# Performance work log

Hardware: AMD Instinct MI355X
Metric: run time of the kernel (lower is better)

The kernel has to match this reference:

```python
import jax, jax.numpy as jnp
import numpy as np


def setup_inputs() -> dict:
    key = jax.random.key(0)
    k1, k2, k3 = jax.random.split(key, 3)
    B, C, H, W = 8, 512, 32, 32
    x = jax.random.normal(k1, (B, C, H, W), dtype=jnp.float32)
    # Conv2d(ch, ch, 3, 1, 1) weights, PyTorch OIHW layout
    fan_in = C * 3 * 3
    weight = jax.random.normal(k2, (C, C, 3, 3), dtype=jnp.float32) / np.sqrt(fan_in)
    bias = jax.random.normal(k3, (C,), dtype=jnp.float32) * 0.01
    return {"x": x, "weight": weight, "bias": bias}


def reference(x, weight, bias):
    up = jnp.repeat(jnp.repeat(x, 2, axis=2), 2, axis=3)
    # Conv3x3, stride 1, padding 1 (same spatial size)
    out = jax.lax.conv_general_dilated(
        up, weight,
        window_strides=(1, 1),
        padding=((1, 1), (1, 1)),
        dimension_numbers=("NCHW", "OIHW", "NCHW"),
    )
    return out + bias[None, :, None, None]
```

## Files before the change

kernel.cpp:

```cpp
#include <hip/hip_runtime.h>
#include <hip/hip_bf16.h>
#include <stdint.h>


typedef __attribute__((ext_vector_type(8)))  __bf16 bf16x8;
typedef __attribute__((ext_vector_type(4)))  float  f32x4;
typedef __attribute__((ext_vector_type(4)))  int    int4v;

__device__ __forceinline__ void async16(const void* g, void* l) {
  __builtin_amdgcn_global_load_lds(
      (const __attribute__((address_space(1))) void*)g,
      (__attribute__((address_space(3))) void*)l,
      16, 0, 0);
}

__global__ void fused_prep(const float* __restrict__ x,
                           const float* __restrict__ w,
                           __hip_bfloat16* __restrict__ xpad,
                           __hip_bfloat16* __restrict__ weff) {
  const int bid = blockIdx.x;
  const int tid = threadIdx.x;
  __shared__ __align__(16) __hip_bfloat16 ldsT[32][80];

  if (bid < 2048) {
    const int blk = bid;
    const int cib = blk & 7;
    const int r   = (blk >> 3) & 31;
    const int b   = blk >> 8;
    const int ci_l = tid >> 2;
    const int wq   = tid & 3;
    const float* xp = x + (((size_t)(b * 512 + cib * 64 + ci_l) * 32 + r) * 32) + wq * 8;
    float4 v0 = *(const float4*)(xp);
    float4 v1 = *(const float4*)(xp + 4);
    const int wb = wq * 8;
    ldsT[wb + 0][ci_l] = __float2bfloat16(v0.x);
    ldsT[wb + 1][ci_l] = __float2bfloat16(v0.y);
    ldsT[wb + 2][ci_l] = __float2bfloat16(v0.z);
    ldsT[wb + 3][ci_l] = __float2bfloat16(v0.w);
    ldsT[wb + 4][ci_l] = __float2bfloat16(v1.x);
    ldsT[wb + 5][ci_l] = __float2bfloat16(v1.y);
    ldsT[wb + 6][ci_l] = __float2bfloat16(v1.z);
    ldsT[wb + 7][ci_l] = __float2bfloat16(v1.w);
    __syncthreads();
    const int w_o = tid >> 3;
    const int ch  = tid & 7;
    char* dst = (char*)xpad +
        ((((size_t)(b * 34 + (r + 1)) * 34) + (w_o + 1)) * 512 + cib * 64 + ch * 8) * 2;
    *(int4v*)dst = *(const int4v*)&ldsT[w_o][ch * 8];
  } else if (bid < 3072) {
    const int idx = (bid - 2048) * 256 + tid;
    const float* wp = w + (size_t)idx * 9;
    const int co = idx >> 9;
    const int ci = idx & 511;
    float t[9];
#pragma unroll
    for (int i = 0; i < 9; ++i) t[i] = wp[i];
#pragma unroll
    for (int py = 0; py < 2; ++py) {
#pragma unroll
      for (int px = 0; px < 2; ++px) {
        const int p = py * 2 + px;
#pragma unroll
        for (int ky = 0; ky < 2; ++ky) {
          const int ulo = (ky == 0) ? 0 : (py == 0 ? 1 : 2);
          const int uhi = (ky == 0) ? (py == 0 ? 0 : 1) : 2;
#pragma unroll
          for (int kx = 0; kx < 2; ++kx) {
            const int vlo = (kx == 0) ? 0 : (px == 0 ? 1 : 2);
            const int vhi = (kx == 0) ? (px == 0 ? 0 : 1) : 2;
            float s = 0.f;
            for (int u = ulo; u <= uhi; ++u)
              for (int v = vlo; v <= vhi; ++v)
                s += t[u * 3 + v];
            const int kk = ky * 2 + kx;
            weff[(((size_t)p * 512 + co) * 4 + kk) * 512 + ci] = __float2bfloat16(s);
          }
        }
      }
    }
  } else if (bid < 3208) {
    const int f  = (bid - 3072) * 2048 + tid * 8;
    const int b  = f / 34816;
    const int rr = (f / 17408) & 1;
    const int off = f % 17408;
    __hip_bfloat16* dst = xpad + ((size_t)(b * 34 + rr * 33) * 17408) + off;
    int4v z = {0, 0, 0, 0};
    *(int4v*)dst = z;
  } else {
    const int f  = (bid - 3208) * 2048 + tid * 8;
    const int b  = f / 32768;
    const int cc = (f / 16384) & 1;
    const int r  = ((f / 512) & 31) + 1;
    const int ci = f & 511;
    __hip_bfloat16* dst = xpad +
        (((size_t)(b * 34 + r) * 34) + cc * 33) * 512 + ci;
    int4v z = {0, 0, 0, 0};
    *(int4v*)dst = z;
  }
}

#define MM(a, b, c) __builtin_amdgcn_mfma_f32_16x16x32_bf16((a), (b), (c), 0, 0, 0)
#define BAR() asm volatile("s_barrier" ::: "memory")
#define PRIO(x) __builtin_amdgcn_s_setprio(x)
#define GATE(N) asm volatile("s_waitcnt vmcnt(" N ")" ::: "memory")

#define ST_A(T, d) do {                                                        \
    char* _l = lds + (d) * 32768 + dA;                                         \
    const __hip_bfloat16* _g = pA0 + (size_t)(T) * 64;                         \
    async16(_g, _l); async16(_g + 131072, _l + 8192);                          \
    async16(_g + 262144, _l + 16384); async16(_g + 393216, _l + 24576);        \
  } while (0)

#define OFFB(T) (((((T) >> 4) * 34) + (((T) >> 3) & 1)) * 512 + ((T) & 7) * 64)
#define ST_B(T, d) do {                                                        \
    char* _l = lds + 65536 + (d) * 32768 + dA;                                 \
    const int _o = OFFB(T);                                                    \
    async16(pB00 + _o, _l); async16(pB01 + _o, _l + 8192);                     \
    async16(pB10 + _o, _l + 16384); async16(pB11 + _o, _l + 24576);            \
  } while (0)

#define RD_A(D, S, mb) do {                                                    \
    _Pragma("unroll") for (int _m = 0; _m < 4; ++_m) {                         \
      (D)[_m * 2]     = *(const bf16x8*)((S) + ((mb) + _m) * 2048 + aoff0);    \
      (D)[_m * 2 + 1] = *(const bf16x8*)((S) + ((mb) + _m) * 2048 + aoff1); }  \
  } while (0)

#define RD_B(D, S, nb) do {                                                    \
    _Pragma("unroll") for (int _n = 0; _n < 2; ++_n) {                         \
      (D)[_n * 2]     = *(const bf16x8*)((S) + ((nb) + _n) * 2048 + aoff0);    \
      (D)[_n * 2 + 1] = *(const bf16x8*)((S) + ((nb) + _n) * 2048 + aoff1); }  \
  } while (0)

#define MFMAQ(mb, nb, A, B) do {                                               \
    _Pragma("unroll") for (int _m = 0; _m < 4; ++_m)                           \
      _Pragma("unroll") for (int _n = 0; _n < 2; ++_n) {                       \
        acc[(mb)+_m][(nb)+_n] = MM((A)[_m*2],   (B)[_n*2],   acc[(mb)+_m][(nb)+_n]); \
        acc[(mb)+_m][(nb)+_n] = MM((A)[_m*2+1], (B)[_n*2+1], acc[(mb)+_m][(nb)+_n]); } \
  } while (0)

#define ITER(T, SE, SO, GE, GO, LAST) do {                                     \
                                                         \
  RD_A(Ab, aS0, 4);                                                            \
  PRIO(1); MFMAQ(0, 0, Aa, Ba); PRIO(0);                                       \
  RD_B(Bb, bS0, 2);                                                            \
  PRIO(1); MFMAQ(4, 0, Ab, Ba); PRIO(0);                                       \
  BAR();                                                                       \
  if (SE) ST_A((T) + 2, 0);                                                    \
  PRIO(1); MFMAQ(4, 2, Ab, Bb); PRIO(0);                                       \
  GATE(GE); BAR();                                                             \
  RD_A(Ab, aS1, 0); RD_B(Ba, bS1, 0);                                          \
  if (SE) ST_B((T) + 2, 0);                                                    \
  PRIO(1); MFMAQ(0, 2, Aa, Bb); PRIO(0);                                       \
                                                          \
  RD_A(Aa, aS1, 4);                                                            \
  PRIO(1); MFMAQ(0, 0, Ab, Ba); PRIO(0);                                       \
  RD_B(Bb, bS1, 2);                                                            \
  PRIO(1); MFMAQ(4, 0, Aa, Ba); PRIO(0);                                       \
  BAR();                                                                       \
  if (SO) ST_A((T) + 3, 1);                                                    \
  PRIO(1); MFMAQ(4, 2, Aa, Bb); PRIO(0);                                       \
  GATE(GO); BAR();                                                             \
  if (!LAST) { RD_A(Aa, aS0, 0); RD_B(Ba, bS0, 0); }                           \
  if (SO) ST_B((T) + 3, 1);                                                    \
  PRIO(1); MFMAQ(0, 2, Ab, Bb); PRIO(0);                                       \
} while (0)

__global__ __launch_bounds__(512, 2) void upconv_gemm(
    const __hip_bfloat16* __restrict__ xpad,
    const __hip_bfloat16* __restrict__ weff,
    const float* __restrict__ bias,
    float* __restrict__ out) {
  extern __shared__ __align__(16) char lds[];

  const int bid = blockIdx.x;
  const int g = bid & 7, i = bid >> 3;
  const int py = g >> 2;
  const int mt = (g >> 1) & 1;
  const int nh = g & 1;
  const int px = i & 1;
  const int nt = nh * 16 + (i >> 1);
  const int p  = py * 2 + px;
  const int co0 = mt << 8;
  const int n0  = nt << 8;
  const int b   = n0 >> 10;
  const int rb  = (n0 & 1023) >> 5;

  const int tid  = threadIdx.x;
  const int lane = tid & 63;
  const int wv   = tid >> 6;
  const int wr   = wv >> 2;
  const int wc   = wv & 3;

  const int srow = tid >> 3;
  const int sl   = (tid & 7) ^ (srow & 7);
  const int dA   = wv * 1024;

  const __hip_bfloat16* wpp = weff + ((size_t)p << 20);
  const __hip_bfloat16* pA0 = wpp + (size_t)(co0 + srow) * 2048 + sl * 8;
  const __hip_bfloat16* pB00 = xpad +
      ((size_t)(b * 34 + rb + (srow >> 5) + py) * 34 + (srow & 31) + px) * 512 + sl * 8;
  const __hip_bfloat16* pB01 = pB00 + (size_t)2 * 34 * 512;
  const __hip_bfloat16* pB10 = pB00 + (size_t)4 * 34 * 512;
  const __hip_bfloat16* pB11 = pB00 + (size_t)6 * 34 * 512;

  const int aoff0 = (lane & 15) * 128 + (((lane >> 4) ^ (lane & 7)) * 16);
  const int aoff1 = (lane & 15) * 128 + ((((lane >> 4) + 4) ^ (lane & 7)) * 16);
  const char* aS0 = lds + wr * 16384;
  const char* aS1 = aS0 + 32768;
  const char* bS0 = lds + 65536 + (wc >> 1) * 16384 + (wc & 1) * 8192;
  const char* bS1 = bS0 + 32768;

  f32x4 acc[8][4] = {};
  bf16x8 Aa[8], Ab[8], Ba[4], Bb[4];

  ST_A(0, 0); ST_B(0, 0);
  ST_A(1, 1); ST_B(1, 1);
  GATE("8"); BAR();
  RD_A(Aa, aS0, 0); RD_B(Ba, bS0, 0);

#pragma unroll 1
  for (int t = 0; t <= 28; t += 2) ITER(t, true, true, "4", "4", false);
  ITER(30, false, false, "0", "0", true);

#pragma unroll
  for (int m = 0; m < 8; ++m) {
    const int coB = co0 + wr * 128 + m * 16 + ((lane >> 4) << 2);
    float bv[4];
#pragma unroll
    for (int j = 0; j < 4; ++j) bv[j] = bias[coB + j];
#pragma unroll
    for (int nn = 0; nn < 4; ++nn) {
      const int nl = wc * 64 + nn * 16 + (lane & 15);
      const int rr = rb + (nl >> 5);
      const int ss = nl & 31;
      const int oh = rr * 2 + py;
      const int ow = ss * 2 + px;
      float* op = out + (((size_t)(b * 512 + coB) << 6) + oh) * 64 + ow;
#pragma unroll
      for (int j = 0; j < 4; ++j)
        op[(size_t)j * 4096] = acc[m][nn][j] + bv[j];
    }
  }
}

extern "C" void kernel_launch(void* const* d_in, const int* in_sizes, int n_in,
                              void* d_out, int out_size, void* d_ws, size_t ws_size,
                              hipStream_t stream) {
  (void)in_sizes; (void)n_in; (void)out_size; (void)ws_size;
  const float* x  = (const float*)d_in[0];
  const float* w  = (const float*)d_in[1];
  const float* bs = (const float*)d_in[2];
  float* out = (float*)d_out;
  char* ws = (char*)d_ws;
  __hip_bfloat16* xpad = (__hip_bfloat16*)ws;
  __hip_bfloat16* weff = (__hip_bfloat16*)(ws + (10u << 20));
  fused_prep<<<dim3(3336), dim3(256), 0, stream>>>(x, w, xpad, weff);
  upconv_gemm<<<dim3(256), dim3(512), 131072, stream>>>(xpad, weff, bs, out);
}
```

Baseline: 75.15 us.

## Shrink GEMM tiles to 128x128 with 256-thread blocks and simpler pipeline

```diff
diff --git a/kernel.cpp b/kernel.cpp
--- a/kernel.cpp
+++ b/kernel.cpp
@@ -105,24 +105,25 @@
 #define GATE(N) asm volatile("s_waitcnt vmcnt(" N ")" ::: "memory")
 
 #define ST_A(T, d) do {                                                        \
-    char* _l = lds + (d) * 32768 + dA;                                         \
+    char* _l = lds + (d) * 16384 + dA;                                         \
     const __hip_bfloat16* _g = pA0 + (size_t)(T) * 64;                         \
-    async16(_g, _l); async16(_g + 131072, _l + 8192);                          \
-    async16(_g + 262144, _l + 16384); async16(_g + 393216, _l + 24576);        \
+    async16(_g, _l);                    async16(_g + 65536, _l + 4096);        \
+    async16(_g + 131072, _l + 8192);    async16(_g + 196608, _l + 12288);      \
   } while (0)
 
 #define OFFB(T) (((((T) >> 4) * 34) + (((T) >> 3) & 1)) * 512 + ((T) & 7) * 64)
 #define ST_B(T, d) do {                                                        \
-    char* _l = lds + 65536 + (d) * 32768 + dA;                                 \
+    char* _l = lds + 32768 + (d) * 16384 + dA;                                 \
     const int _o = OFFB(T);                                                    \
-    async16(pB00 + _o, _l); async16(pB01 + _o, _l + 8192);                     \
-    async16(pB10 + _o, _l + 16384); async16(pB11 + _o, _l + 24576);            \
-  } while (0)
-
-#define RD_A(D, S, mb) do {                                                    \
+    async16(pB0 + _o, _l);               async16(pB0 + _o + 17408, _l + 4096); \
+    async16(pB0 + _o + 34816, _l + 8192);                                      \
+    async16(pB0 + _o + 52224, _l + 12288);                                     \
+  } while (0)
+
+#define RD_A(D, S) do {                                                        \
     _Pragma("unroll") for (int _m = 0; _m < 4; ++_m) {                         \
-      (D)[_m * 2]     = *(const bf16x8*)((S) + ((mb) + _m) * 2048 + aoff0);    \
-      (D)[_m * 2 + 1] = *(const bf16x8*)((S) + ((mb) + _m) * 2048 + aoff1); }  \
+      (D)[_m * 2]     = *(const bf16x8*)((S) + _m * 2048 + aoff0);             \
+      (D)[_m * 2 + 1] = *(const bf16x8*)((S) + _m * 2048 + aoff1); }           \
   } while (0)
 
 #define RD_B(D, S, nb) do {                                                    \
@@ -131,41 +132,31 @@
       (D)[_n * 2 + 1] = *(const bf16x8*)((S) + ((nb) + _n) * 2048 + aoff1); }  \
   } while (0)
 
-#define MFMAQ(mb, nb, A, B) do {                                               \
+#define MFMAQ(A, B, nb) do {                                                   \
     _Pragma("unroll") for (int _m = 0; _m < 4; ++_m)                           \
       _Pragma("unroll") for (int _n = 0; _n < 2; ++_n) {                       \
-        acc[(mb)+_m][(nb)+_n] = MM((A)[_m*2],   (B)[_n*2],   acc[(mb)+_m][(nb)+_n]); \
-        acc[(mb)+_m][(nb)+_n] = MM((A)[_m*2+1], (B)[_n*2+1], acc[(mb)+_m][(nb)+_n]); } \
-  } while (0)
-
-#define ITER(T, SE, SO, GE, GO, LAST) do {                                     \
-                                                         \
-  RD_A(Ab, aS0, 4);                                                            \
-  PRIO(1); MFMAQ(0, 0, Aa, Ba); PRIO(0);                                       \
+        acc[_m][(nb)+_n] = MM((A)[_m*2],   (B)[_n*2],   acc[_m][(nb)+_n]);     \
+        acc[_m][(nb)+_n] = MM((A)[_m*2+1], (B)[_n*2+1], acc[_m][(nb)+_n]); }   \
+  } while (0)
+
+#define ITER(T, SE, SO, LAST) do {                                             \
+                                                       \
   RD_B(Bb, bS0, 2);                                                            \
-  PRIO(1); MFMAQ(4, 0, Ab, Ba); PRIO(0);                                       \
-  BAR();                                                                       \
-  if (SE) ST_A((T) + 2, 0);                                                    \
-  PRIO(1); MFMAQ(4, 2, Ab, Bb); PRIO(0);                                       \
-  GATE(GE); BAR();                                                             \
-  RD_A(Ab, aS1, 0); RD_B(Ba, bS1, 0);                                          \
-  if (SE) ST_B((T) + 2, 0);                                                    \
-  PRIO(1); MFMAQ(0, 2, Aa, Bb); PRIO(0);                                       \
-                                                          \
-  RD_A(Aa, aS1, 4);                                                            \
-  PRIO(1); MFMAQ(0, 0, Ab, Ba); PRIO(0);                                       \
+  PRIO(1); MFMAQ(Aa, Ba, 0); PRIO(0);                                          \
+  GATE("0"); BAR();                                                            \
+  if (SE) { ST_A((T) + 2, 0); ST_B((T) + 2, 0); }                              \
+  RD_A(Ab, aS1); RD_B(Ba, bS1, 0);                                             \
+  PRIO(1); MFMAQ(Aa, Bb, 2); PRIO(0);                                          \
+                                                      \
   RD_B(Bb, bS1, 2);                                                            \
-  PRIO(1); MFMAQ(4, 0, Aa, Ba); PRIO(0);                                       \
-  BAR();                                                                       \
-  if (SO) ST_A((T) + 3, 1);                                                    \
-  PRIO(1); MFMAQ(4, 2, Aa, Bb); PRIO(0);                                       \
-  GATE(GO); BAR();                                                             \
-  if (!LAST) { RD_A(Aa, aS0, 0); RD_B(Ba, bS0, 0); }                           \
-  if (SO) ST_B((T) + 3, 1);                                                    \
-  PRIO(1); MFMAQ(0, 2, Ab, Bb); PRIO(0);                                       \
+  PRIO(1); MFMAQ(Ab, Ba, 0); PRIO(0);                                          \
+  GATE("0"); BAR();                                                            \
+  if (SO) { ST_A((T) + 3, 1); ST_B((T) + 3, 1); }                              \
+  if (!LAST) { RD_A(Aa, aS0); RD_B(Ba, bS0, 0); }                              \
+  PRIO(1); MFMAQ(Ab, Bb, 2); PRIO(0);                                          \
 } while (0)
 
-__global__ __launch_bounds__(512, 2) void upconv_gemm(
+__global__ __launch_bounds__(256, 2) void upconv_gemm(
     const __hip_bfloat16* __restrict__ xpad,
     const __hip_bfloat16* __restrict__ weff,
     const float* __restrict__ bias,
@@ -175,56 +166,51 @@
   const int bid = blockIdx.x;
   const int g = bid & 7, i = bid >> 3;
   const int py = g >> 2;
-  const int mt = (g >> 1) & 1;
-  const int nh = g & 1;
+  const int mt = g & 3;
   const int px = i & 1;
-  const int nt = nh * 16 + (i >> 1);
+  const int nt = i >> 1;
   const int p  = py * 2 + px;
-  const int co0 = mt << 8;
-  const int n0  = nt << 8;
-  const int b   = n0 >> 10;
-  const int rb  = (n0 & 1023) >> 5;
+  const int co0 = mt << 7;
+  const int b   = nt >> 3;
+  const int rb  = (nt & 7) << 2;
 
   const int tid  = threadIdx.x;
   const int lane = tid & 63;
   const int wv   = tid >> 6;
-  const int wr   = wv >> 2;
-  const int wc   = wv & 3;
+  const int wr   = wv >> 1;
+  const int wc   = wv & 1;
 
   const int srow = tid >> 3;
   const int sl   = (tid & 7) ^ (srow & 7);
   const int dA   = wv * 1024;
 
-  const __hip_bfloat16* wpp = weff + ((size_t)p << 20);
-  const __hip_bfloat16* pA0 = wpp + (size_t)(co0 + srow) * 2048 + sl * 8;
-  const __hip_bfloat16* pB00 = xpad +
-      ((size_t)(b * 34 + rb + (srow >> 5) + py) * 34 + (srow & 31) + px) * 512 + sl * 8;
-  const __hip_bfloat16* pB01 = pB00 + (size_t)2 * 34 * 512;
-  const __hip_bfloat16* pB10 = pB00 + (size_t)4 * 34 * 512;
-  const __hip_bfloat16* pB11 = pB00 + (size_t)6 * 34 * 512;
+  const __hip_bfloat16* pA0 = weff + ((size_t)p << 20)
+      + (size_t)(co0 + srow) * 2048 + sl * 8;
+  const __hip_bfloat16* pB0 = xpad +
+      ((size_t)(b * 34 + rb + py) * 34 + srow + px) * 512 + sl * 8;
 
   const int aoff0 = (lane & 15) * 128 + (((lane >> 4) ^ (lane & 7)) * 16);
   const int aoff1 = (lane & 15) * 128 + ((((lane >> 4) + 4) ^ (lane & 7)) * 16);
-  const char* aS0 = lds + wr * 16384;
-  const char* aS1 = aS0 + 32768;
-  const char* bS0 = lds + 65536 + (wc >> 1) * 16384 + (wc & 1) * 8192;
-  const char* bS1 = bS0 + 32768;
-
-  f32x4 acc[8][4] = {};
+  const char* aS0 = lds + wr * 8192;
+  const char* aS1 = aS0 + 16384;
+  const char* bS0 = lds + 32768 + wc * 8192;
+  const char* bS1 = bS0 + 16384;
+
+  f32x4 acc[4][4] = {};
   bf16x8 Aa[8], Ab[8], Ba[4], Bb[4];
 
   ST_A(0, 0); ST_B(0, 0);
   ST_A(1, 1); ST_B(1, 1);
   GATE("8"); BAR();
-  RD_A(Aa, aS0, 0); RD_B(Ba, bS0, 0);
+  RD_A(Aa, aS0); RD_B(Ba, bS0, 0);
 
 #pragma unroll 1
-  for (int t = 0; t <= 28; t += 2) ITER(t, true, true, "4", "4", false);
-  ITER(30, false, false, "0", "0", true);
-
-#pragma unroll
-  for (int m = 0; m < 8; ++m) {
-    const int coB = co0 + wr * 128 + m * 16 + ((lane >> 4) << 2);
+  for (int t = 0; t <= 28; t += 2) ITER(t, true, true, false);
+  ITER(30, false, false, true);
+
+#pragma unroll
+  for (int m = 0; m < 4; ++m) {
+    const int coB = co0 + wr * 64 + m * 16 + ((lane >> 4) << 2);
     float bv[4];
 #pragma unroll
     for (int j = 0; j < 4; ++j) bv[j] = bias[coB + j];
@@ -255,5 +241,5 @@
   __hip_bfloat16* xpad = (__hip_bfloat16*)ws;
   __hip_bfloat16* weff = (__hip_bfloat16*)(ws + (10u << 20));
   fused_prep<<<dim3(3336), dim3(256), 0, stream>>>(x, w, xpad, weff);
-  upconv_gemm<<<dim3(256), dim3(512), 131072, stream>>>(xpad, weff, bs, out);
-}
+  upconv_gemm<<<dim3(1024), dim3(256), 65536, stream>>>(xpad, weff, bs, out);
+}
```

After: 83.35 us. 10.9% more time.

## Stagger wave roles: read-first and MFMA-first schedules per wave row

Applied to the files above, without the earlier changes.

```diff
diff --git a/kernel.cpp b/kernel.cpp
--- a/kernel.cpp
+++ b/kernel.cpp
@@ -138,7 +138,7 @@
         acc[(mb)+_m][(nb)+_n] = MM((A)[_m*2+1], (B)[_n*2+1], acc[(mb)+_m][(nb)+_n]); } \
   } while (0)
 
-#define ITER(T, SE, SO, GE, GO, LAST) do {                                     \
+#define ITER_RF(T, SE, SO, GE, GO, LAST) do {                                  \
                                                          \
   RD_A(Ab, aS0, 4);                                                            \
   PRIO(1); MFMAQ(0, 0, Aa, Ba); PRIO(0);                                       \
@@ -163,6 +163,33 @@
   if (!LAST) { RD_A(Aa, aS0, 0); RD_B(Ba, bS0, 0); }                           \
   if (SO) ST_B((T) + 3, 1);                                                    \
   PRIO(1); MFMAQ(0, 2, Ab, Bb); PRIO(0);                                       \
+} while (0)
+
+#define ITER_MF(T, SE, SO, GE, GO, LAST) do {                                  \
+                                                         \
+  PRIO(1); MFMAQ(0, 0, Aa, Ba); PRIO(0);                                       \
+  RD_A(Ab, aS0, 4);                                                            \
+  PRIO(1); MFMAQ(4, 0, Ab, Ba); PRIO(0);                                       \
+  RD_B(Bb, bS0, 2);                                                            \
+  BAR();                                                                       \
+  PRIO(1); MFMAQ(4, 2, Ab, Bb); PRIO(0);                                       \
+  if (SE) ST_A((T) + 2, 0);                                                    \
+  GATE(GE); BAR();                                                             \
+  PRIO(1); MFMAQ(0, 2, Aa, Bb); PRIO(0);                                       \
+  RD_A(Ab, aS1, 0); RD_B(Ba, bS1, 0);                                          \
+  if (SE) ST_B((T) + 2, 0);                                                    \
+                                                          \
+  PRIO(1); MFMAQ(0, 0, Ab, Ba); PRIO(0);                                       \
+  RD_A(Aa, aS1, 4);                                                            \
+  PRIO(1); MFMAQ(4, 0, Aa, Ba); PRIO(0);                                       \
+  RD_B(Bb, bS1, 2);                                                            \
+  BAR();                                                                       \
+  PRIO(1); MFMAQ(4, 2, Aa, Bb); PRIO(0);                                       \
+  if (SO) ST_A((T) + 3, 1);                                                    \
+  GATE(GO); BAR();                                                             \
+  PRIO(1); MFMAQ(0, 2, Ab, Bb); PRIO(0);                                       \
+  if (!LAST) { RD_A(Aa, aS0, 0); RD_B(Ba, bS0, 0); }                           \
+  if (SO) ST_B((T) + 3, 1);                                                    \
 } while (0)
 
 __global__ __launch_bounds__(512, 2) void upconv_gemm(
@@ -218,9 +245,15 @@
   GATE("8"); BAR();
   RD_A(Aa, aS0, 0); RD_B(Ba, bS0, 0);
 
+  if (wr == 0) {
 #pragma unroll 1
-  for (int t = 0; t <= 28; t += 2) ITER(t, true, true, "4", "4", false);
-  ITER(30, false, false, "0", "0", true);
+    for (int t = 0; t <= 28; t += 2) ITER_RF(t, true, true, "4", "4", false);
+    ITER_RF(30, false, false, "0", "0", true);
+  } else {
+#pragma unroll 1
+    for (int t = 0; t <= 28; t += 2) ITER_MF(t, true, true, "4", "4", false);
+    ITER_MF(30, false, false, "0", "0", true);
+  }
 
 #pragma unroll
   for (int m = 0; m < 8; ++m) {
```

Result: no change. 74.52 us (-0.8%).

## Load B operand fragments directly from global into registers, bypassing LDS

Applied to the files above, without the earlier changes.

```diff
diff --git a/kernel.cpp b/kernel.cpp
--- a/kernel.cpp
+++ b/kernel.cpp
@@ -112,12 +112,6 @@
   } while (0)
 
 #define OFFB(T) (((((T) >> 4) * 34) + (((T) >> 3) & 1)) * 512 + ((T) & 7) * 64)
-#define ST_B(T, d) do {                                                        \
-    char* _l = lds + 65536 + (d) * 32768 + dA;                                 \
-    const int _o = OFFB(T);                                                    \
-    async16(pB00 + _o, _l); async16(pB01 + _o, _l + 8192);                     \
-    async16(pB10 + _o, _l + 16384); async16(pB11 + _o, _l + 24576);            \
-  } while (0)
 
 #define RD_A(D, S, mb) do {                                                    \
     _Pragma("unroll") for (int _m = 0; _m < 4; ++_m) {                         \
@@ -125,10 +119,11 @@
       (D)[_m * 2 + 1] = *(const bf16x8*)((S) + ((mb) + _m) * 2048 + aoff1); }  \
   } while (0)
 
-#define RD_B(D, S, nb) do {                                                    \
+#define RD_BG(D, T, nb) do {                                                   \
     _Pragma("unroll") for (int _n = 0; _n < 2; ++_n) {                         \
-      (D)[_n * 2]     = *(const bf16x8*)((S) + ((nb) + _n) * 2048 + aoff0);    \
-      (D)[_n * 2 + 1] = *(const bf16x8*)((S) + ((nb) + _n) * 2048 + aoff1); }  \
+      const __hip_bfloat16* _p = pB[(nb) + _n] + OFFB(T);                      \
+      (D)[_n * 2]     = *(const bf16x8*)(_p);                                  \
+      (D)[_n * 2 + 1] = *(const bf16x8*)(_p + 32); }                           \
   } while (0)
 
 #define MFMAQ(mb, nb, A, B) do {                                               \
@@ -139,29 +134,29 @@
   } while (0)
 
 #define ITER(T, SE, SO, GE, GO, LAST) do {                                     \
-                                                         \
+                                                       \
   RD_A(Ab, aS0, 4);                                                            \
   PRIO(1); MFMAQ(0, 0, Aa, Ba); PRIO(0);                                       \
-  RD_B(Bb, bS0, 2);                                                            \
+  RD_BG(Bb, (T), 2);                                                           \
   PRIO(1); MFMAQ(4, 0, Ab, Ba); PRIO(0);                                       \
   BAR();                                                                       \
+  RD_BG(Ba, (T) + 1, 0);                                                       \
   if (SE) ST_A((T) + 2, 0);                                                    \
   PRIO(1); MFMAQ(4, 2, Ab, Bb); PRIO(0);                                       \
   GATE(GE); BAR();                                                             \
-  RD_A(Ab, aS1, 0); RD_B(Ba, bS1, 0);                                          \
-  if (SE) ST_B((T) + 2, 0);                                                    \
+  RD_A(Ab, aS1, 0);                                                            \
   PRIO(1); MFMAQ(0, 2, Aa, Bb); PRIO(0);                                       \
-                                                          \
+                                                      \
   RD_A(Aa, aS1, 4);                                                            \
   PRIO(1); MFMAQ(0, 0, Ab, Ba); PRIO(0);                                       \
-  RD_B(Bb, bS1, 2);                                                            \
+  RD_BG(Bb, (T) + 1, 2);                                                       \
   PRIO(1); MFMAQ(4, 0, Aa, Ba); PRIO(0);                                       \
   BAR();                                                                       \
+  if (!LAST) RD_BG(Ba, (T) + 2, 0);                                            \
   if (SO) ST_A((T) + 3, 1);                                                    \
   PRIO(1); MFMAQ(4, 2, Aa, Bb); PRIO(0);                                       \
   GATE(GO); BAR();                                                             \
-  if (!LAST) { RD_A(Aa, aS0, 0); RD_B(Ba, bS0, 0); }                           \
-  if (SO) ST_B((T) + 3, 1);                                                    \
+  if (!LAST) RD_A(Aa, aS0, 0);                                                 \
   PRIO(1); MFMAQ(0, 2, Ab, Bb); PRIO(0);                                       \
 } while (0)
 
@@ -195,32 +190,34 @@
   const int sl   = (tid & 7) ^ (srow & 7);
   const int dA   = wv * 1024;
 
-  const __hip_bfloat16* wpp = weff + ((size_t)p << 20);
-  const __hip_bfloat16* pA0 = wpp + (size_t)(co0 + srow) * 2048 + sl * 8;
-  const __hip_bfloat16* pB00 = xpad +
-      ((size_t)(b * 34 + rb + (srow >> 5) + py) * 34 + (srow & 31) + px) * 512 + sl * 8;
-  const __hip_bfloat16* pB01 = pB00 + (size_t)2 * 34 * 512;
-  const __hip_bfloat16* pB10 = pB00 + (size_t)4 * 34 * 512;
-  const __hip_bfloat16* pB11 = pB00 + (size_t)6 * 34 * 512;
+  const __hip_bfloat16* pA0 = weff + ((size_t)p << 20)
+      + (size_t)(co0 + srow) * 2048 + sl * 8;
+
+  const __hip_bfloat16* pB[4];
+#pragma unroll
+  for (int nn = 0; nn < 4; ++nn) {
+    const int n = wc * 64 + nn * 16 + (lane & 15);
+    const int r = n >> 5, s = n & 31;
+    pB[nn] = xpad + ((size_t)(b * 34 + rb + r + py) * 34 + s + px) * 512
+           + (lane >> 4) * 8;
+  }
 
   const int aoff0 = (lane & 15) * 128 + (((lane >> 4) ^ (lane & 7)) * 16);
   const int aoff1 = (lane & 15) * 128 + ((((lane >> 4) + 4) ^ (lane & 7)) * 16);
   const char* aS0 = lds + wr * 16384;
   const char* aS1 = aS0 + 32768;
-  const char* bS0 = lds + 65536 + (wc >> 1) * 16384 + (wc & 1) * 8192;
-  const char* bS1 = bS0 + 32768;
 
   f32x4 acc[8][4] = {};
   bf16x8 Aa[8], Ab[8], Ba[4], Bb[4];
 
-  ST_A(0, 0); ST_B(0, 0);
-  ST_A(1, 1); ST_B(1, 1);
-  GATE("8"); BAR();
-  RD_A(Aa, aS0, 0); RD_B(Ba, bS0, 0);
+  RD_BG(Ba, 0, 0);
+  ST_A(0, 0); ST_A(1, 1);
+  GATE("4"); BAR();
+  RD_A(Aa, aS0, 0);
 
 #pragma unroll 1
-  for (int t = 0; t <= 28; t += 2) ITER(t, true, true, "4", "4", false);
-  ITER(30, false, false, "0", "0", true);
+  for (int t = 0; t <= 28; t += 2) ITER(t, true, true, "8", "8", false);
+  ITER(30, false, false, "8", "0", true);
 
 #pragma unroll
   for (int m = 0; m < 8; ++m) {
@@ -255,5 +252,5 @@
   __hip_bfloat16* xpad = (__hip_bfloat16*)ws;
   __hip_bfloat16* weff = (__hip_bfloat16*)(ws + (10u << 20));
   fused_prep<<<dim3(3336), dim3(256), 0, stream>>>(x, w, xpad, weff);
-  upconv_gemm<<<dim3(256), dim3(512), 131072, stream>>>(xpad, weff, bs, out);
-}
+  upconv_gemm<<<dim3(256), dim3(512), 65536, stream>>>(xpad, weff, bs, out);
+}
```

After: 114.1 us. 1.52x slower.
